# Performance work log

Hardware: AMD Instinct MI355X
Metric: run time of the kernel (lower is better)

## Reference

```python
import jax, jax.numpy as jnp
import numpy as np

B, Cfi, H, W = 2, 32, 192, 192
Cfp, Cfo, NUM = 1, 2, 16
N = H * W
Ct = Cfo + Cfi + Cfi + Cfp  # 67
EPS = 1e-5


def _bn(x, g, b, m, v):
    # x: (B, C, num, N); per-channel inference batchnorm
    inv = g * jax.lax.rsqrt(v + EPS)
    return x * inv[None, :, None, None] + (b - m * inv)[None, :, None, None]


def _pconv(x, Wt):
    # 1x1 conv as channel contraction: Wt (Cout, Cin), x (B, Cin, num, N)
    return jnp.einsum('oc,bcmn->bomn', Wt, x)


def setup_inputs() -> dict:
    key = jax.random.key(0)
    ks = jax.random.split(key, 32)
    inp = {
        'If': jax.random.normal(ks[0], (B, Cfi, H, W), jnp.float32),
        'Pf': jax.random.normal(ks[1], (B, Cfp, H, W), jnp.float32),
        'Ofnum': jax.random.normal(ks[2], (B, Cfo, NUM, N), jnp.float32),
        'args': jax.random.randint(ks[3], (B, NUM, N), 0, N, jnp.int64),
    }
    def conv_w(k, co, ci):
        return jax.random.normal(k, (co, ci), jnp.float32) * (1.0 / np.sqrt(ci))
    def bn_p(k, c):
        k1, k2 = jax.random.split(k)
        return (jnp.ones((c,), jnp.float32),
                jnp.zeros((c,), jnp.float32),
                jax.random.normal(k1, (c,), jnp.float32) * 0.1,
                jax.random.uniform(k2, (c,), jnp.float32, 0.5, 1.5))
    # convXF: Ct->Cfi, Cfi->Cfi (both BN+GELU)
    inp['W1'] = conv_w(ks[4], Cfi, Ct)
    inp['g1'], inp['b1'], inp['m1'], inp['v1'] = bn_p(ks[5], Cfi)
    inp['W2'] = conv_w(ks[6], Cfi, Cfi)
    inp['g2'], inp['b2'], inp['m2'], inp['v2'] = bn_p(ks[7], Cfi)
    # convXL: Cfi->Cfi (BN+GELU), Cfi->Cfi (BN only)
    inp['W3'] = conv_w(ks[8], Cfi, Cfi)
    inp['g3'], inp['b3'], inp['m3'], inp['v3'] = bn_p(ks[9], Cfi)
    inp['W4'] = conv_w(ks[10], Cfi, Cfi)
    inp['g4'], inp['b4'], inp['m4'], inp['v4'] = bn_p(ks[11], Cfi)
    # coef: Cfi -> 3, with bias
    inp['Wc'] = conv_w(ks[12], 3, Cfi)
    inp['bc'] = jax.random.normal(ks[13], (3,), jnp.float32) * 0.01
    return inp


def reference(If, Pf, Ofnum, args,
              W1, g1, b1, m1, v1,
              W2, g2, b2, m2, v2,
              W3, g3, b3, m3, v3,
              W4, g4, b4, m4, v4,
              Wc, bc):
    gelu = lambda x: jax.nn.gelu(x, approximate=False)
    If_flat = If.reshape(B, Cfi, N)   # (B, Cfi, N)
    Pf_flat = Pf.reshape(B, Cfp, N)   # (B, Cfp, M), M == N here

    # per-batch neighbor gather along flattened spatial dim
    gath = jax.vmap(lambda f, a: f[:, a])  # (C,N),(num,N) -> (C,num,N)
    IPfnum = gath(If_flat, args)            # (B, Cfi, num, N)
    Pfnum = gath(Pf_flat, args)             # (B, Cfp, num, N)
    Ifnum = jnp.broadcast_to(If_flat[:, :, None, :], (B, Cfi, NUM, N))

    X = jnp.concatenate([Ifnum, IPfnum, Pfnum, Ofnum], axis=1)  # (B, Ct, num, N)

    h = gelu(_bn(_pconv(X, W1), g1, b1, m1, v1))
    h = gelu(_bn(_pconv(h, W2), g2, b2, m2, v2))
    l = gelu(_bn(_pconv(h, W3), g3, b3, m3, v3))
    l = _bn(_pconv(l, W4), g4, b4, m4, v4)
    XF = gelu(h + l)

    feat = _pconv(XF, Wc) + bc[None, :, None, None]  # (B, 3, num, N)
    Alpha, Beta, Omega = feat[:, 0:1], feat[:, 1:2], feat[:, 2:3]
    Omega = jax.nn.softmax(Omega, axis=2)
    dout = jnp.sum(((Alpha + 1.0) * Pfnum[:, -1:] + Beta) * Omega,
                   axis=2, keepdims=True)  # (B, 1, 1, N)
    return dout.reshape(B, 1, H, W)
```

## Files before the change

### kernel.cpp

```cpp
#include <hip/hip_runtime.h>
#include <math.h>

#define BB   2
#define CFI  32
#define NN   36864
#define NUMM 16

#define ZOFSU (BB * NN * 16)

typedef __attribute__((ext_vector_type(8))) short short8;
typedef __attribute__((ext_vector_type(4))) float f4;
typedef __attribute__((ext_vector_type(16))) float f16v;
typedef __attribute__((ext_vector_type(4))) unsigned uint4v;
typedef __attribute__((ext_vector_type(2))) unsigned u2v;

static __device__ __forceinline__ f16v mm32(short8 a, short8 b, f16v c) {
    return __builtin_amdgcn_mfma_f32_32x32x16_bf16(a, b, c, 0, 0, 0);
}

template <int CTRL>
static __device__ __forceinline__ float dpp_add(float x) {
    int y = __builtin_amdgcn_update_dpp(0, __builtin_bit_cast(int, x),
                                        CTRL, 0xf, 0xf, true);
    return x + __builtin_bit_cast(float, y);
}
template <int CTRL>
static __device__ __forceinline__ float dpp_max(float x) {
    int y = __builtin_amdgcn_update_dpp(0, __builtin_bit_cast(int, x),
                                        CTRL, 0xf, 0xf, true);
    return fmaxf(x, __builtin_bit_cast(float, y));
}

static __device__ __forceinline__ float gelu_fast(float x) {
    const float x2  = x * x;
    const float q   = fmaf(-0.10294310f, x2, -2.30211813f);
    const float e   = exp2f(q * x);
    const float r   = __builtin_amdgcn_rcpf(e + 1.0f);
    return x * r;
}

static __device__ __forceinline__ unsigned bf16_rne_bits(float x) {
    unsigned u = __builtin_bit_cast(unsigned, x);
    return u + 0x7fffu + ((u >> 16) & 1u);
}
static __device__ __forceinline__ void split_pack(float x0, float x1,
                                                  unsigned& hi, unsigned& lo) {
    unsigned r0 = bf16_rne_bits(x0);
    unsigned r1 = bf16_rne_bits(x1);
    float h0 = __builtin_bit_cast(float, r0 & 0xffff0000u);
    float h1 = __builtin_bit_cast(float, r1 & 0xffff0000u);
    hi = (r0 >> 16) | (r1 & 0xffff0000u);
    unsigned s0 = bf16_rne_bits(x0 - h0);
    unsigned s1 = bf16_rne_bits(x1 - h1);
    lo = (s0 >> 16) | (s1 & 0xffff0000u);
}

static __device__ __forceinline__ unsigned pack2(float a, float b) {
    unsigned ua = __builtin_bit_cast(unsigned, a) + 0x8000u;
    unsigned ub = __builtin_bit_cast(unsigned, b) + 0x8000u;
    return (ua >> 16) | (ub & 0xffff0000u);
}
static __device__ __forceinline__ float bflo(unsigned u) {
    return __builtin_bit_cast(float, u << 16);
}
static __device__ __forceinline__ float bfhi(unsigned u) {
    return __builtin_bit_cast(float, u & 0xffff0000u);
}

union UV { unsigned u[4]; short8 v; };

__global__ __launch_bounds__(256) void yz_kernel(
    const float* __restrict__ If, const float* __restrict__ Pf,
    const float* __restrict__ W1, const float* __restrict__ g1,
    const float* __restrict__ b1, const float* __restrict__ m1,
    const float* __restrict__ v1,
    float* __restrict__ wsYZ)
{
    __shared__ float wy[1024], wz[1024], wp[32], bt1[32];
    for (int i = threadIdx.x; i < 1024; i += 256) {
        int o = i >> 5, c = i & 31;
        float inv = g1[o] * rsqrtf(v1[o] + 1e-5f);
        wy[i] = W1[o * 67 + c]      * inv;
        wz[i] = W1[o * 67 + 32 + c] * inv;
    }
    if (threadIdx.x < 32) {
        int o = threadIdx.x;
        float inv = g1[o] * rsqrtf(v1[o] + 1e-5f);
        wp[o]  = W1[o * 67 + 64] * inv;
        bt1[o] = b1[o] - m1[o] * inv;
    }
    __syncthreads();

    const int r  = threadIdx.x & 3;
    const int p  = blockIdx.x * 64 + (threadIdx.x >> 2);
    const int b  = p / NN, n = p - b * NN;
    const int o0 = r * 8;
    const float* ifp = If + (size_t)b * CFI * NN + n;

    float v[32];
#pragma unroll
    for (int c = 0; c < 32; c++) v[c] = ifp[(size_t)c * NN];
    const float pf = Pf[p];

    float accY[8], accZ[8];
#pragma unroll
    for (int j = 0; j < 8; j++) {
        const float4* wyr = (const float4*)&wy[(o0 + j) * 32];
        const float4* wzr = (const float4*)&wz[(o0 + j) * 32];
        float ay = bt1[o0 + j];
        float az = wp[o0 + j] * pf;
#pragma unroll
        for (int c4 = 0; c4 < 8; c4++) {
            float4 a = wyr[c4], z = wzr[c4];
            ay = fmaf(a.x, v[4 * c4 + 0], ay);  az = fmaf(z.x, v[4 * c4 + 0], az);
            ay = fmaf(a.y, v[4 * c4 + 1], ay);  az = fmaf(z.y, v[4 * c4 + 1], az);
            ay = fmaf(a.z, v[4 * c4 + 2], ay);  az = fmaf(z.z, v[4 * c4 + 2], az);
            ay = fmaf(a.w, v[4 * c4 + 3], ay);  az = fmaf(z.w, v[4 * c4 + 3], az);
        }
        accY[j] = ay; accZ[j] = az;
    }

    unsigned* wsu = (unsigned*)wsYZ;
    u2v yA, yB, zA, zB;
    yA[0] = pack2(accY[0], accY[1]); yA[1] = pack2(accY[2], accY[3]);
    yB[0] = pack2(accY[4], accY[5]); yB[1] = pack2(accY[6], accY[7]);
    zA[0] = pack2(accZ[0], accZ[1]); zA[1] = pack2(accZ[2], accZ[3]);
    zB[0] = pack2(accZ[4], accZ[5]); zB[1] = pack2(accZ[6], accZ[7]);
    *(u2v*)(wsu + (size_t)p * 16 + 2 * r)          = yA;
    *(u2v*)(wsu + (size_t)p * 16 + 8 + 2 * r)      = yB;
    *(u2v*)(wsu + ZOFSU + (size_t)p * 16 + 2 * r)     = zA;
    *(u2v*)(wsu + ZOFSU + (size_t)p * 16 + 8 + 2 * r) = zB;
}

#define LOADL(Lc)                                                             \
    {                                                                         \
        A0l = *(const short8*)&wfrag[(Lc)][0][1][lane + io][0];               \
        A0h = *(const short8*)&wfrag[(Lc)][0][0][lane + io][0];               \
        A1l = *(const short8*)&wfrag[(Lc)][1][1][lane + io][0];               \
        A1h = *(const short8*)&wfrag[(Lc)][1][0][lane + io][0];               \
        bq0 = *(const f4*)&btl[(Lc) * 32 +      4 * hi + 4 * io];             \
        bq1 = *(const f4*)&btl[(Lc) * 32 +  8 + 4 * hi + 4 * io];             \
        bq2 = *(const f4*)&btl[(Lc) * 32 + 16 + 4 * hi + 4 * io];             \
        bq3 = *(const f4*)&btl[(Lc) * 32 + 24 + 4 * hi + 4 * io];             \
    }

#define LAYER_MM(ACCV, BIN0, BIN1)                                            \
    {                                                                         \
        ACCV[0]  = bq0[0]; ACCV[1]  = bq0[1]; ACCV[2]  = bq0[2]; ACCV[3]  = bq0[3]; \
        ACCV[4]  = bq1[0]; ACCV[5]  = bq1[1]; ACCV[6]  = bq1[2]; ACCV[7]  = bq1[3]; \
        ACCV[8]  = bq2[0]; ACCV[9]  = bq2[1]; ACCV[10] = bq2[2]; ACCV[11] = bq2[3]; \
        ACCV[12] = bq3[0]; ACCV[13] = bq3[1]; ACCV[14] = bq3[2]; ACCV[15] = bq3[3]; \
        ACCV = mm32(A0l, BIN0.v, ACCV);                                       \
        ACCV = mm32(A0h, BIN0.v, ACCV);                                       \
        ACCV = mm32(A1l, BIN1.v, ACCV);                                       \
        ACCV = mm32(A1h, BIN1.v, ACCV);                                       \
    }

#define GELU_PACK(ACCV, B0V, B1V)                                             \
    {                                                                         \
        _Pragma("unroll")                                                     \
        for (int k = 0; k < 4; k++) {                                         \
            float t0 = gelu_fast(ACCV[2 * k]);                                \
            float t1 = gelu_fast(ACCV[2 * k + 1]);                            \
            B0V.u[k] = pack2(t0, t1);                                         \
            float t2 = gelu_fast(ACCV[8 + 2 * k]);                            \
            float t3 = gelu_fast(ACCV[8 + 2 * k + 1]);                        \
            B1V.u[k] = pack2(t2, t3);                                         \
        }                                                                     \
    }

__global__ __launch_bounds__(256, 5) void main_kernel(
    const float* __restrict__ Pf, const float* __restrict__ Of,
    const int* __restrict__ args,
    const float* __restrict__ W1, const float* __restrict__ g1,
    const float* __restrict__ v1,
    const float* __restrict__ W2, const float* __restrict__ g2,
    const float* __restrict__ b2, const float* __restrict__ m2,
    const float* __restrict__ v2,
    const float* __restrict__ W3, const float* __restrict__ g3,
    const float* __restrict__ b3, const float* __restrict__ m3,
    const float* __restrict__ v3,
    const float* __restrict__ W4, const float* __restrict__ g4,
    const float* __restrict__ b4, const float* __restrict__ m4,
    const float* __restrict__ v4,
    const float* __restrict__ Wc, const float* __restrict__ bc,
    const float* __restrict__ ws, float* __restrict__ out)
{
    __shared__ __align__(16) unsigned wfrag[3][2][2][64][4];
    __shared__ __align__(16) float btl[3 * 32];
    __shared__ __align__(16) float wch[3 * 32];
    __shared__ __align__(16) float w1t[2 * 32];
    __shared__ float bcs[3];
    __shared__ int   izs;

    const float* Ws[3] = {W2, W3, W4};
    const float* gs[3] = {g2, g3, g4};
    const float* vs[3] = {v2, v3, v4};
    const float* bs[3] = {b2, b3, b4};
    const float* ms[3] = {m2, m3, m4};

    for (int idx = threadIdx.x; idx < 1536; idx += 256) {
        int pp  = idx & 3;
        int ln  = (idx >> 2) & 63;
        int kh  = (idx >> 8) & 1;
        int L   = idx >> 9;
        int row = ln & 31;
        int g   = ln >> 5;
        int k   = kh * 16 + 4 * g + 2 * (pp & 1) + 8 * (pp >> 1);
        float inv = gs[L][row] * rsqrtf(vs[L][row] + 1e-5f);
        float w0 = Ws[L][row * 32 + k]     * inv;
        float w1 = Ws[L][row * 32 + k + 1] * inv;
        unsigned hiw, low;
        split_pack(w0, w1, hiw, low);
        wfrag[L][kh][0][ln][pp] = hiw;
        wfrag[L][kh][1][ln][pp] = low;
    }
    if (threadIdx.x < 96) {
        int L = threadIdx.x >> 5, ch = threadIdx.x & 31;
        btl[threadIdx.x] = bs[L][ch] - ms[L][ch] * (gs[L][ch] * rsqrtf(vs[L][ch] + 1e-5f));
        wch[threadIdx.x] = Wc[L * 32 + ch];
    }
    if (threadIdx.x < 64) {
        int t = threadIdx.x >> 5, ch = threadIdx.x & 31;
        float i1 = g1[ch] * rsqrtf(v1[ch] + 1e-5f);
        w1t[threadIdx.x] = W1[ch * 67 + 65 + t] * i1;
    }
    if (threadIdx.x < 3) bcs[threadIdx.x] = bc[threadIdx.x];
    if (threadIdx.x == 0) izs = (int)(args[0] >> 16);
    __syncthreads();

    const unsigned* wsu = (const unsigned*)ws;
    const int lane  = threadIdx.x & 63;
    const int wid   = threadIdx.x >> 6;
    const int m     = lane & 15;
    const int pt    = (lane >> 4) & 1;
    const int hi    = lane >> 5;
    const int q4    = hi << 2;
    const int izero = izs;

    const int base  = blockIdx.x * 32 + wid * 8 + pt;

    uint4v yu0, yu1, zu0, zu1;
    float of0v, of1v, pfg_n;
    int   aI_n;
    {
        const int C0 = base;
        const int b0 = (C0 >= NN) ? 1 : 0;
        const int n0 = C0 - b0 * NN;
        const int a0 = args[(b0 * NUMM + m) * NN + n0];
        of0v = Of[((b0 * 2 + 0) * NUMM + m) * NN + n0];
        of1v = Of[((b0 * 2 + 1) * NUMM + m) * NN + n0];
        pfg_n = Pf[b0 * NN + a0];
        const uint4v* yb = (const uint4v*)(wsu + (size_t)(b0 * NN + n0) * 16 + hi * 8);
        const uint4v* zb = (const uint4v*)(wsu + ZOFSU + (size_t)(b0 * NN + a0) * 16 + hi * 8);
        yu0 = yb[0]; yu1 = yb[1];
        zu0 = zb[0]; zu1 = zb[1];
        const int C1 = (C0 + 2 < BB * NN) ? C0 + 2 : BB * NN - 1;
        const int b1_ = (C1 >= NN) ? 1 : 0;
        const int n1_ = C1 - b1_ * NN;
        aI_n = args[(b1_ * NUMM + m) * NN + n1_];
    }

#pragma unroll 1
    for (int i = 0; i < 4; i++) {
        const int io = i & izero;
        const int C  = base + i * 2;
        const int b  = (C >= NN) ? 1 : 0;
        const int n  = C - b * NN;
        const float pfg = pfg_n;

        short8 A0l, A0h, A1l, A1h;
        f4 bq0, bq1, bq2, bq3;
        LOADL(0);

        UV B0, B1;
#pragma unroll
        for (int q = 0; q < 4; q++) {
            const f4 waq = *(const f4*)&w1t[8 * q + q4 + 4 * io];
            const f4 wbq = *(const f4*)&w1t[32 + 8 * q + q4 + 4 * io];
            const unsigned ya0 = (q < 2) ? yu0[2 * q]     : yu1[2 * q - 4];
            const unsigned ya1 = (q < 2) ? yu0[2 * q + 1] : yu1[2 * q - 3];
            const unsigned za0 = (q < 2) ? zu0[2 * q]     : zu1[2 * q - 4];
            const unsigned za1 = (q < 2) ? zu0[2 * q + 1] : zu1[2 * q - 3];
            float t0 = fmaf(of1v, wbq[0], fmaf(of0v, waq[0], bflo(ya0) + bflo(za0)));
            float t1 = fmaf(of1v, wbq[1], fmaf(of0v, waq[1], bfhi(ya0) + bfhi(za0)));
            float t2 = fmaf(of1v, wbq[2], fmaf(of0v, waq[2], bflo(ya1) + bflo(za1)));
            float t3 = fmaf(of1v, wbq[3], fmaf(of0v, waq[3], bfhi(ya1) + bfhi(za1)));
            t0 = gelu_fast(t0); t1 = gelu_fast(t1);
            t2 = gelu_fast(t2); t3 = gelu_fast(t3);
            const unsigned lo2 = pack2(t0, t1), hi2 = pack2(t2, t3);
            if (q < 2) { B0.u[2 * q] = lo2; B0.u[2 * q + 1] = hi2; }
            else       { B1.u[2 * q - 4] = lo2; B1.u[2 * q - 3] = hi2; }
        }

        {
            const int Cn = (C + 2 < BB * NN) ? C + 2 : BB * NN - 1;
            const int bn = (Cn >= NN) ? 1 : 0;
            const int nn = Cn - bn * NN;
            const uint4v* ybn = (const uint4v*)(wsu + (size_t)(bn * NN + nn) * 16 + hi * 8);
            yu0 = ybn[0]; yu1 = ybn[1];
            of0v = Of[((bn * 2 + 0) * NUMM + m) * NN + nn];
            of1v = Of[((bn * 2 + 1) * NUMM + m) * NN + nn];
            const int aN = aI_n;
            pfg_n = Pf[bn * NN + aN];
            const uint4v* zbn = (const uint4v*)(wsu + ZOFSU + (size_t)(bn * NN + aN) * 16 + hi * 8);
            zu0 = zbn[0]; zu1 = zbn[1];
            const int Ca = (C + 4 < BB * NN) ? C + 4 : BB * NN - 1;
            const int ba = (Ca >= NN) ? 1 : 0;
            const int na = Ca - ba * NN;
            aI_n = args[(ba * NUMM + m) * NN + na];
        }

        f16v acc;
        LAYER_MM(acc, B0, B1);
        LOADL(1);
        UV P0, P1;
        GELU_PACK(acc, P0, P1);
        B0 = P0; B1 = P1;

        LAYER_MM(acc, B0, B1);
        LOADL(2);
        GELU_PACK(acc, B0, B1);

        LAYER_MM(acc, B0, B1);

        float pa = 0.0f, pb = 0.0f, po = 0.0f;
#pragma unroll
        for (int q = 0; q < 4; q++) {
            const f4 wAq = *(const f4*)&wch[      8 * q + q4 + 4 * io];
            const f4 wBq = *(const f4*)&wch[32 +  8 * q + q4 + 4 * io];
            const f4 wOq = *(const f4*)&wch[64 +  8 * q + q4 + 4 * io];
            const unsigned pu0 = (q < 2) ? P0.u[2 * q]     : P1.u[2 * q - 4];
            const unsigned pu1 = (q < 2) ? P0.u[2 * q + 1] : P1.u[2 * q - 3];
            const float h20 = bflo(pu0), h21 = bfhi(pu0);
            const float h22 = bflo(pu1), h23 = bfhi(pu1);
            float xf0 = gelu_fast(h20 + acc[4 * q + 0]);
            float xf1 = gelu_fast(h21 + acc[4 * q + 1]);
            float xf2 = gelu_fast(h22 + acc[4 * q + 2]);
            float xf3 = gelu_fast(h23 + acc[4 * q + 3]);
            pa = fmaf(wAq[0], xf0, pa); pa = fmaf(wAq[1], xf1, pa);
            pa = fmaf(wAq[2], xf2, pa); pa = fmaf(wAq[3], xf3, pa);
            pb = fmaf(wBq[0], xf0, pb); pb = fmaf(wBq[1], xf1, pb);
            pb = fmaf(wBq[2], xf2, pb); pb = fmaf(wBq[3], xf3, pb);
            po = fmaf(wOq[0], xf0, po); po = fmaf(wOq[1], xf1, po);
            po = fmaf(wOq[2], xf2, po); po = fmaf(wOq[3], xf3, po);
        }
        pa += __shfl_xor(pa, 32, 64);
        pb += __shfl_xor(pb, 32, 64);
        po += __shfl_xor(po, 32, 64);

        const float alpha = pa + bcs[0];
        const float beta_ = pb + bcs[1];
        const float omega = po + bcs[2];
        const float val = fmaf(alpha + 1.0f, pfg, beta_);

        float mx = dpp_max<0xB1>(omega);
        mx = dpp_max<0x4E>(mx);
        mx = dpp_max<0x141>(mx);
        mx = dpp_max<0x140>(mx);
        const float e = __expf(omega - mx);
        float S = e, T = val * e;
        S = dpp_add<0xB1>(S);   T = dpp_add<0xB1>(T);
        S = dpp_add<0x4E>(S);   T = dpp_add<0x4E>(T);
        S = dpp_add<0x141>(S);  T = dpp_add<0x141>(T);
        S = dpp_add<0x140>(S);  T = dpp_add<0x140>(T);

        if ((lane & 15) == 0 && lane < 32)
            out[b * NN + n] = T * __builtin_amdgcn_rcpf(S);
    }
}

extern "C" void kernel_launch(void* const* d_in, const int* in_sizes, int n_in,
                              void* d_out, int out_size, void* d_ws, size_t ws_size,
                              hipStream_t stream) {
    const float* If    = (const float*)d_in[0];
    const float* Pf    = (const float*)d_in[1];
    const float* Of    = (const float*)d_in[2];
    const int*   args  = (const int*)d_in[3];
    const float* W1    = (const float*)d_in[4];
    const float* g1    = (const float*)d_in[5];
    const float* b1    = (const float*)d_in[6];
    const float* m1    = (const float*)d_in[7];
    const float* v1    = (const float*)d_in[8];
    const float* W2    = (const float*)d_in[9];
    const float* g2    = (const float*)d_in[10];
    const float* b2    = (const float*)d_in[11];
    const float* m2    = (const float*)d_in[12];
    const float* v2    = (const float*)d_in[13];
    const float* W3    = (const float*)d_in[14];
    const float* g3    = (const float*)d_in[15];
    const float* b3    = (const float*)d_in[16];
    const float* m3    = (const float*)d_in[17];
    const float* v3    = (const float*)d_in[18];
    const float* W4    = (const float*)d_in[19];
    const float* g4    = (const float*)d_in[20];
    const float* b4    = (const float*)d_in[21];
    const float* m4    = (const float*)d_in[22];
    const float* v4    = (const float*)d_in[23];
    const float* Wc    = (const float*)d_in[24];
    const float* bc    = (const float*)d_in[25];

    float* ws  = (float*)d_ws;
    float* out = (float*)d_out;

    yz_kernel<<<(BB * NN) / 64, 256, 0, stream>>>(
        If, Pf, W1, g1, b1, m1, v1, ws);

    main_kernel<<<(BB * NN) / 32, 256, 0, stream>>>(
        Pf, Of, args,
        W1, g1, v1,
        W2, g2, b2, m2, v2,
        W3, g3, b3, m3, v3,
        W4, g4, b4, m4, v4,
        Wc, bc, ws, out);
}
```

Before: 225.7 us.

## Split layer-1 gather and GELU into separate kernel writing bf16 activations to workspace

Adds an h1_kernel that performs the neighbor gather (args, Of, Pf, Y/Z partial sums), applies the first layer's GELU, and writes the packed bf16 h1 activations plus the gathered Pf to workspace. A new main_kernel2 then streams these contiguous activations instead of doing the scattered gather inline. The goal is to take the irregular gather latency out of the MFMA-heavy main kernel. In exchange it adds an extra launch and a large write and read-back of h1 (about 4.7MB each way). It falls back to the old fused path when the workspace is too small.

```diff
diff --git a/kernel.cpp b/kernel.cpp
--- a/kernel.cpp
+++ b/kernel.cpp
@@ -7,6 +7,10 @@
 #define NUMM 16
 
 #define ZOFSU (BB * NN * 16)
+#define H1OFS (2 * BB * NN * 16)
+#define H1SZ  (BB * NN * 16 * 16)
+#define PFOFS (H1OFS + H1SZ)
+#define WS_NEEDED_BYTES ((size_t)(PFOFS + BB * NN * 16) * 4)
 
 typedef __attribute__((ext_vector_type(8))) short short8;
 typedef __attribute__((ext_vector_type(4))) float f4;
@@ -132,6 +136,70 @@
     *(u2v*)(wsu + ZOFSU + (size_t)p * 16 + 8 + 2 * r) = zB;
 }
 
+__global__ __launch_bounds__(256) void h1_kernel(
+    const float* __restrict__ Pf, const float* __restrict__ Of,
+    const int* __restrict__ args,
+    const float* __restrict__ W1, const float* __restrict__ g1,
+    const float* __restrict__ v1,
+    float* __restrict__ wsF)
+{
+    __shared__ float w1a[32], w1b[32];
+    if (threadIdx.x < 64) {
+        int t = threadIdx.x >> 5, ch = threadIdx.x & 31;
+        float i1 = g1[ch] * rsqrtf(v1[ch] + 1e-5f);
+        float w = W1[ch * 67 + 65 + t] * i1;
+        if (t == 0) w1a[ch] = w; else w1b[ch] = w;
+    }
+    __syncthreads();
+
+    unsigned* wsu = (unsigned*)wsF;
+    const int m = threadIdx.x & 15;
+    const int p = blockIdx.x * 16 + (threadIdx.x >> 4);
+    const int b = (p >= NN) ? 1 : 0;
+    const int n = p - b * NN;
+
+    const int   a   = args[(b * NUMM + m) * NN + n];
+    const float of0 = Of[((b * 2 + 0) * NUMM + m) * NN + n];
+    const float of1 = Of[((b * 2 + 1) * NUMM + m) * NN + n];
+    const float pfg = Pf[b * NN + a];
+
+    const uint4v* yb = (const uint4v*)(wsu + (size_t)p * 16);
+    const uint4v* zb = (const uint4v*)(wsu + ZOFSU + (size_t)(b * NN + a) * 16);
+    uint4v yv0 = yb[0], yv1 = yb[1], yv2 = yb[2], yv3 = yb[3];
+    uint4v zv0 = zb[0], zv1 = zb[1], zv2 = zb[2], zv3 = zb[3];
+
+    unsigned outv[16];
+#pragma unroll
+    for (int u = 0; u < 16; u += 2) {
+        const int hi = u >> 3, q = (u & 7) >> 1;
+        const int c  = 8 * q + 4 * hi;
+        const f4 wa = *(const f4*)&w1a[c];
+        const f4 wb = *(const f4*)&w1b[c];
+        const unsigned yu0 = (u < 4) ? yv0[u & 3] : (u < 8) ? yv1[u & 3]
+                           : (u < 12) ? yv2[u & 3] : yv3[u & 3];
+        const unsigned yu1 = ((u + 1) < 4) ? yv0[(u + 1) & 3] : ((u + 1) < 8) ? yv1[(u + 1) & 3]
+                           : ((u + 1) < 12) ? yv2[(u + 1) & 3] : yv3[(u + 1) & 3];
+        const unsigned zu0 = (u < 4) ? zv0[u & 3] : (u < 8) ? zv1[u & 3]
+                           : (u < 12) ? zv2[u & 3] : zv3[u & 3];
+        const unsigned zu1 = ((u + 1) < 4) ? zv0[(u + 1) & 3] : ((u + 1) < 8) ? zv1[(u + 1) & 3]
+                           : ((u + 1) < 12) ? zv2[(u + 1) & 3] : zv3[(u + 1) & 3];
+        float x0 = fmaf(of1, wb[0], fmaf(of0, wa[0], bflo(yu0) + bflo(zu0)));
+        float x1 = fmaf(of1, wb[1], fmaf(of0, wa[1], bfhi(yu0) + bfhi(zu0)));
+        float x2 = fmaf(of1, wb[2], fmaf(of0, wa[2], bflo(yu1) + bflo(zu1)));
+        float x3 = fmaf(of1, wb[3], fmaf(of0, wa[3], bfhi(yu1) + bfhi(zu1)));
+        outv[u]     = pack2(gelu_fast(x0), gelu_fast(x1));
+        outv[u + 1] = pack2(gelu_fast(x2), gelu_fast(x3));
+    }
+
+    uint4v* op = (uint4v*)(wsu + H1OFS + ((size_t)p * 16 + m) * 16);
+    uint4v o0, o1, o2, o3;
+#pragma unroll
+    for (int k = 0; k < 4; k++) { o0[k] = outv[k]; o1[k] = outv[4 + k];
+                                  o2[k] = outv[8 + k]; o3[k] = outv[12 + k]; }
+    op[0] = o0; op[1] = o1; op[2] = o2; op[3] = o3;
+    wsF[PFOFS + (size_t)p * 16 + m] = pfg;
+}
+
 #define LOADL(Lc)                                                             \
     {                                                                         \
         A0l = *(const short8*)&wfrag[(Lc)][0][1][lane + io][0];               \
@@ -168,6 +236,160 @@
             B1V.u[k] = pack2(t2, t3);                                         \
         }                                                                     \
     }
+
+#define MAIN_PROLOGUE                                                         \
+    const float* Ws[3] = {W2, W3, W4};                                        \
+    const float* gs[3] = {g2, g3, g4};                                        \
+    const float* vs[3] = {v2, v3, v4};                                        \
+    const float* bs[3] = {b2, b3, b4};                                        \
+    const float* ms[3] = {m2, m3, m4};                                        \
+    for (int idx = threadIdx.x; idx < 1536; idx += 256) {                     \
+        int pp  = idx & 3;                                                    \
+        int ln  = (idx >> 2) & 63;                                            \
+        int kh  = (idx >> 8) & 1;                                             \
+        int L   = idx >> 9;                                                   \
+        int row = ln & 31;                                                    \
+        int g   = ln >> 5;                                                    \
+        int k   = kh * 16 + 4 * g + 2 * (pp & 1) + 8 * (pp >> 1);             \
+        float inv = gs[L][row] * rsqrtf(vs[L][row] + 1e-5f);                  \
+        float w0 = Ws[L][row * 32 + k]     * inv;                             \
+        float w1 = Ws[L][row * 32 + k + 1] * inv;                             \
+        unsigned hiw, low;                                                    \
+        split_pack(w0, w1, hiw, low);                                         \
+        wfrag[L][kh][0][ln][pp] = hiw;                                        \
+        wfrag[L][kh][1][ln][pp] = low;                                        \
+    }                                                                         \
+    if (threadIdx.x < 96) {                                                   \
+        int L = threadIdx.x >> 5, ch = threadIdx.x & 31;                      \
+        btl[threadIdx.x] = bs[L][ch] - ms[L][ch] * (gs[L][ch] * rsqrtf(vs[L][ch] + 1e-5f)); \
+        wch[threadIdx.x] = Wc[L * 32 + ch];                                   \
+    }                                                                         \
+    if (threadIdx.x < 3) bcs[threadIdx.x] = bc[threadIdx.x];
+
+__global__ __launch_bounds__(256, 5) void main_kernel2(
+    const int* __restrict__ args,
+    const float* __restrict__ W2, const float* __restrict__ g2,
+    const float* __restrict__ b2, const float* __restrict__ m2,
+    const float* __restrict__ v2,
+    const float* __restrict__ W3, const float* __restrict__ g3,
+    const float* __restrict__ b3, const float* __restrict__ m3,
+    const float* __restrict__ v3,
+    const float* __restrict__ W4, const float* __restrict__ g4,
+    const float* __restrict__ b4, const float* __restrict__ m4,
+    const float* __restrict__ v4,
+    const float* __restrict__ Wc, const float* __restrict__ bc,
+    const float* __restrict__ ws, float* __restrict__ out)
+{
+    __shared__ __align__(16) unsigned wfrag[3][2][2][64][4];
+    __shared__ __align__(16) float btl[3 * 32];
+    __shared__ __align__(16) float wch[3 * 32];
+    __shared__ float bcs[3];
+    __shared__ int   izs;
+
+    MAIN_PROLOGUE
+    if (threadIdx.x == 0) izs = (int)(args[0] >> 16);
+    __syncthreads();
+
+    const unsigned* wsu = (const unsigned*)ws;
+    const unsigned* h1g = wsu + H1OFS;
+    const float*    pff = ws + PFOFS;
+    const int lane  = threadIdx.x & 63;
+    const int wid   = threadIdx.x >> 6;
+    const int m     = lane & 15;
+    const int pt    = (lane >> 4) & 1;
+    const int hi    = lane >> 5;
+    const int q4    = hi << 2;
+    const int izero = izs;
+
+    const int base  = blockIdx.x * 32 + wid * 8 + pt;
+
+    uint4v h0c, h1c;
+    float pfg_n;
+    {
+        const unsigned* hp = h1g + ((size_t)base * 16 + m) * 16 + hi * 8;
+        h0c = *(const uint4v*)hp;
+        h1c = *(const uint4v*)(hp + 4);
+        pfg_n = pff[(size_t)base * 16 + m];
+    }
+
+#pragma unroll 1
+    for (int i = 0; i < 4; i++) {
+        const int io = i & izero;
+        const int C  = base + i * 2;
+        const float pfg = pfg_n;
+
+        short8 A0l, A0h, A1l, A1h;
+        f4 bq0, bq1, bq2, bq3;
+        LOADL(0);
+
+        UV B0, B1;
+#pragma unroll
+        for (int k = 0; k < 4; k++) { B0.u[k] = h0c[k]; B1.u[k] = h1c[k]; }
+
+        {
+            const int Cn = (C + 2 < BB * NN) ? C + 2 : BB * NN - 1;
+            const unsigned* hp = h1g + ((size_t)Cn * 16 + m) * 16 + hi * 8;
+            h0c = *(const uint4v*)hp;
+            h1c = *(const uint4v*)(hp + 4);
+            pfg_n = pff[(size_t)Cn * 16 + m];
+        }
+
+        f16v acc;
+        LAYER_MM(acc, B0, B1);
+        LOADL(1);
+        UV P0, P1;
+        GELU_PACK(acc, P0, P1);
+        B0 = P0; B1 = P1;
+
+        LAYER_MM(acc, B0, B1);
+        LOADL(2);
+        GELU_PACK(acc, B0, B1);
+
+        LAYER_MM(acc, B0, B1);
+
+        float pa = 0.0f, pb = 0.0f, po = 0.0f;
+#pragma unroll
+        for (int q = 0; q < 4; q++) {
+            const f4 wAq = *(const f4*)&wch[      8 * q + q4 + 4 * io];
+            const f4 wBq = *(const f4*)&wch[32 +  8 * q + q4 + 4 * io];
+            const f4 wOq = *(const f4*)&wch[64 +  8 * q + q4 + 4 * io];
+            const unsigned pu0 = (q < 2) ? P0.u[2 * q]     : P1.u[2 * q - 4];
+            const unsigned pu1 = (q < 2) ? P0.u[2 * q + 1] : P1.u[2 * q - 3];
+            float xf0 = gelu_fast(bflo(pu0) + acc[4 * q + 0]);
+            float xf1 = gelu_fast(bfhi(pu0) + acc[4 * q + 1]);
+            float xf2 = gelu_fast(bflo(pu1) + acc[4 * q + 2]);
+            float xf3 = gelu_fast(bfhi(pu1) + acc[4 * q + 3]);
+            pa = fmaf(wAq[0], xf0, pa); pa = fmaf(wAq[1], xf1, pa);
+            pa = fmaf(wAq[2], xf2, pa); pa = fmaf(wAq[3], xf3, pa);
+            pb = fmaf(wBq[0], xf0, pb); pb = fmaf(wBq[1], xf1, pb);
+            pb = fmaf(wBq[2], xf2, pb); pb = fmaf(wBq[3], xf3, pb);
+            po = fmaf(wOq[0], xf0, po); po = fmaf(wOq[1], xf1, po);
+            po = fmaf(wOq[2], xf2, po); po = fmaf(wOq[3], xf3, po);
+        }
+        pa += __shfl_xor(pa, 32, 64);
+        pb += __shfl_xor(pb, 32, 64);
+        po += __shfl_xor(po, 32, 64);
+
+        const float alpha = pa + bcs[0];
+        const float beta_ = pb + bcs[1];
+        const float omega = po + bcs[2];
+        const float val = fmaf(alpha + 1.0f, pfg, beta_);
+
+        float mx = dpp_max<0xB1>(omega);
+        mx = dpp_max<0x4E>(mx);
+        mx = dpp_max<0x141>(mx);
+        mx = dpp_max<0x140>(mx);
+        const float e = __expf(omega - mx);
+        float S = e, T = val * e;
+        S = dpp_add<0xB1>(S);   T = dpp_add<0xB1>(T);
+        S = dpp_add<0x4E>(S);   T = dpp_add<0x4E>(T);
+        S = dpp_add<0x141>(S);  T = dpp_add<0x141>(T);
+        S = dpp_add<0x140>(S);  T = dpp_add<0x140>(T);
+
+        if ((lane & 15) == 0 && lane < 32)
+            out[C] = T * __builtin_amdgcn_rcpf(S);
+    }
+}
 
 __global__ __launch_bounds__(256, 5) void main_kernel(
     const float* __restrict__ Pf, const float* __restrict__ Of,
@@ -193,39 +415,12 @@
     __shared__ float bcs[3];
     __shared__ int   izs;
 
-    const float* Ws[3] = {W2, W3, W4};
-    const float* gs[3] = {g2, g3, g4};
-    const float* vs[3] = {v2, v3, v4};
-    const float* bs[3] = {b2, b3, b4};
-    const float* ms[3] = {m2, m3, m4};
-
-    for (int idx = threadIdx.x; idx < 1536; idx += 256) {
-        int pp  = idx & 3;
-        int ln  = (idx >> 2) & 63;
-        int kh  = (idx >> 8) & 1;
-        int L   = idx >> 9;
-        int row = ln & 31;
-        int g   = ln >> 5;
-        int k   = kh * 16 + 4 * g + 2 * (pp & 1) + 8 * (pp >> 1);
-        float inv = gs[L][row] * rsqrtf(vs[L][row] + 1e-5f);
-        float w0 = Ws[L][row * 32 + k]     * inv;
-        float w1 = Ws[L][row * 32 + k + 1] * inv;
-        unsigned hiw, low;
-        split_pack(w0, w1, hiw, low);
-        wfrag[L][kh][0][ln][pp] = hiw;
-        wfrag[L][kh][1][ln][pp] = low;
-    }
-    if (threadIdx.x < 96) {
-        int L = threadIdx.x >> 5, ch = threadIdx.x & 31;
-        btl[threadIdx.x] = bs[L][ch] - ms[L][ch] * (gs[L][ch] * rsqrtf(vs[L][ch] + 1e-5f));
-        wch[threadIdx.x] = Wc[L * 32 + ch];
-    }
+    MAIN_PROLOGUE
     if (threadIdx.x < 64) {
         int t = threadIdx.x >> 5, ch = threadIdx.x & 31;
         float i1 = g1[ch] * rsqrtf(v1[ch] + 1e-5f);
         w1t[threadIdx.x] = W1[ch * 67 + 65 + t] * i1;
     }
-    if (threadIdx.x < 3) bcs[threadIdx.x] = bc[threadIdx.x];
     if (threadIdx.x == 0) izs = (int)(args[0] >> 16);
     __syncthreads();
 
@@ -332,12 +527,10 @@
             const f4 wOq = *(const f4*)&wch[64 +  8 * q + q4 + 4 * io];
             const unsigned pu0 = (q < 2) ? P0.u[2 * q]     : P1.u[2 * q - 4];
             const unsigned pu1 = (q < 2) ? P0.u[2 * q + 1] : P1.u[2 * q - 3];
-            const float h20 = bflo(pu0), h21 = bfhi(pu0);
-            const float h22 = bflo(pu1), h23 = bfhi(pu1);
-            float xf0 = gelu_fast(h20 + acc[4 * q + 0]);
-            float xf1 = gelu_fast(h21 + acc[4 * q + 1]);
-            float xf2 = gelu_fast(h22 + acc[4 * q + 2]);
-            float xf3 = gelu_fast(h23 + acc[4 * q + 3]);
+            float xf0 = gelu_fast(bflo(pu0) + acc[4 * q + 0]);
+            float xf1 = gelu_fast(bfhi(pu0) + acc[4 * q + 1]);
+            float xf2 = gelu_fast(bflo(pu1) + acc[4 * q + 2]);
+            float xf3 = gelu_fast(bfhi(pu1) + acc[4 * q + 3]);
             pa = fmaf(wAq[0], xf0, pa); pa = fmaf(wAq[1], xf1, pa);
             pa = fmaf(wAq[2], xf2, pa); pa = fmaf(wAq[3], xf3, pa);
             pb = fmaf(wBq[0], xf0, pb); pb = fmaf(wBq[1], xf1, pb);
@@ -406,11 +599,22 @@
     yz_kernel<<<(BB * NN) / 64, 256, 0, stream>>>(
         If, Pf, W1, g1, b1, m1, v1, ws);
 
-    main_kernel<<<(BB * NN) / 32, 256, 0, stream>>>(
-        Pf, Of, args,
-        W1, g1, v1,
-        W2, g2, b2, m2, v2,
-        W3, g3, b3, m3, v3,
-        W4, g4, b4, m4, v4,
-        Wc, bc, ws, out);
-}
+    if (ws_size >= WS_NEEDED_BYTES) {
+        h1_kernel<<<(BB * NN) / 16, 256, 0, stream>>>(
+            Pf, Of, args, W1, g1, v1, ws);
+        main_kernel2<<<(BB * NN) / 32, 256, 0, stream>>>(
+            args,
+            W2, g2, b2, m2, v2,
+            W3, g3, b3, m3, v3,
+            W4, g4, b4, m4, v4,
+            Wc, bc, ws, out);
+    } else {
+        main_kernel<<<(BB * NN) / 32, 256, 0, stream>>>(
+            Pf, Of, args,
+            W1, g1, v1,
+            W2, g2, b2, m2, v2,
+            W3, g3, b3, m3, v3,
+            W4, g4, b4, m4, v4,
+            Wc, bc, ws, out);
+    }
+}
```

After: 245.1 us. 1.09x slower.

## Split first-layer gather and GELU into a separate kernel staging bf16 activations

Applied to the files above, without the earlier changes.

Adds an h1_kernel that gathers the Y/Z partial sums, Of and Pf per neighbor, applies the first layer's BN and GELU, and writes packed bf16 activations plus the gathered Pf values to workspace. The main kernel then reads these precomputed activations instead of doing the irregular gathers and layer-1 math inline. It also runs at a higher occupancy hint (6) and loads bias values inside the layer macro. The aim is to lighten the MFMA kernel and cut its register pressure. In exchange it adds a large workspace write and re-read of the intermediate activations, and it relies on the workspace being big enough, which is never checked.

```diff
diff --git a/kernel.cpp b/kernel.cpp
--- a/kernel.cpp
+++ b/kernel.cpp
@@ -7,6 +7,10 @@
 #define NUMM 16
 
 #define ZOFSU (BB * NN * 16)
+#define H1OFS (2 * BB * NN * 16)
+#define H1SZ  (BB * NN * 16 * 16)
+#define PFOFS (H1OFS + H1SZ)
+#define WS_NEEDED_BYTES ((size_t)(PFOFS + BB * NN * 16) * 4)
 
 typedef __attribute__((ext_vector_type(8))) short short8;
 typedef __attribute__((ext_vector_type(4))) float f4;
@@ -132,24 +136,80 @@
     *(u2v*)(wsu + ZOFSU + (size_t)p * 16 + 8 + 2 * r) = zB;
 }
 
+__global__ __launch_bounds__(256) void h1_kernel(
+    const float* __restrict__ Pf, const float* __restrict__ Of,
+    const int* __restrict__ args,
+    const float* __restrict__ W1, const float* __restrict__ g1,
+    const float* __restrict__ v1,
+    float* __restrict__ wsF)
+{
+    __shared__ float w1a[32], w1b[32];
+    if (threadIdx.x < 64) {
+        int t = threadIdx.x >> 5, ch = threadIdx.x & 31;
+        float i1 = g1[ch] * rsqrtf(v1[ch] + 1e-5f);
+        float w = W1[ch * 67 + 65 + t] * i1;
+        if (t == 0) w1a[ch] = w; else w1b[ch] = w;
+    }
+    __syncthreads();
+
+    unsigned* wsu = (unsigned*)wsF;
+    const int qd = threadIdx.x & 3;
+    const int m  = (threadIdx.x >> 2) & 15;
+    const int p  = blockIdx.x * 4 + (threadIdx.x >> 6);
+    const int b  = (p >= NN) ? 1 : 0;
+    const int n  = p - b * NN;
+
+    const int   a   = args[(b * NUMM + m) * NN + n];
+    const float of0 = Of[((b * 2 + 0) * NUMM + m) * NN + n];
+    const float of1 = Of[((b * 2 + 1) * NUMM + m) * NN + n];
+
+    const uint4v y16 = *(const uint4v*)(wsu + (size_t)p * 16 + qd * 4);
+    const uint4v z16 = *(const uint4v*)(wsu + ZOFSU + (size_t)(b * NN + a) * 16 + qd * 4);
+
+    const int c_a = (qd & 1) * 16 + (qd >> 1) * 4;
+    const f4 waA = *(const f4*)&w1a[c_a];
+    const f4 wbA = *(const f4*)&w1b[c_a];
+    const f4 waB = *(const f4*)&w1a[c_a + 8];
+    const f4 wbB = *(const f4*)&w1b[c_a + 8];
+
+    float x0 = fmaf(of1, wbA[0], fmaf(of0, waA[0], bflo(y16[0]) + bflo(z16[0])));
+    float x1 = fmaf(of1, wbA[1], fmaf(of0, waA[1], bfhi(y16[0]) + bfhi(z16[0])));
+    float x2 = fmaf(of1, wbA[2], fmaf(of0, waA[2], bflo(y16[1]) + bflo(z16[1])));
+    float x3 = fmaf(of1, wbA[3], fmaf(of0, waA[3], bfhi(y16[1]) + bfhi(z16[1])));
+    float x4 = fmaf(of1, wbB[0], fmaf(of0, waB[0], bflo(y16[2]) + bflo(z16[2])));
+    float x5 = fmaf(of1, wbB[1], fmaf(of0, waB[1], bfhi(y16[2]) + bfhi(z16[2])));
+    float x6 = fmaf(of1, wbB[2], fmaf(of0, waB[2], bflo(y16[3]) + bflo(z16[3])));
+    float x7 = fmaf(of1, wbB[3], fmaf(of0, waB[3], bfhi(y16[3]) + bfhi(z16[3])));
+
+    uint4v o;
+    o[0] = pack2(gelu_fast(x0), gelu_fast(x1));
+    o[1] = pack2(gelu_fast(x2), gelu_fast(x3));
+    o[2] = pack2(gelu_fast(x4), gelu_fast(x5));
+    o[3] = pack2(gelu_fast(x6), gelu_fast(x7));
+
+    *(uint4v*)(wsu + H1OFS + ((size_t)p * 16 + m) * 16 + qd * 4) = o;
+    if (qd == 0) wsF[PFOFS + (size_t)p * 16 + m] = Pf[b * NN + a];
+}
+
 #define LOADL(Lc)                                                             \
     {                                                                         \
         A0l = *(const short8*)&wfrag[(Lc)][0][1][lane + io][0];               \
         A0h = *(const short8*)&wfrag[(Lc)][0][0][lane + io][0];               \
         A1l = *(const short8*)&wfrag[(Lc)][1][1][lane + io][0];               \
         A1h = *(const short8*)&wfrag[(Lc)][1][0][lane + io][0];               \
-        bq0 = *(const f4*)&btl[(Lc) * 32 +      4 * hi + 4 * io];             \
-        bq1 = *(const f4*)&btl[(Lc) * 32 +  8 + 4 * hi + 4 * io];             \
-        bq2 = *(const f4*)&btl[(Lc) * 32 + 16 + 4 * hi + 4 * io];             \
-        bq3 = *(const f4*)&btl[(Lc) * 32 + 24 + 4 * hi + 4 * io];             \
-    }
-
-#define LAYER_MM(ACCV, BIN0, BIN1)                                            \
+    }
+
+#define LAYER_MM(Lc, ACCV, BIN0, BIN1)                                        \
     {                                                                         \
-        ACCV[0]  = bq0[0]; ACCV[1]  = bq0[1]; ACCV[2]  = bq0[2]; ACCV[3]  = bq0[3]; \
-        ACCV[4]  = bq1[0]; ACCV[5]  = bq1[1]; ACCV[6]  = bq1[2]; ACCV[7]  = bq1[3]; \
-        ACCV[8]  = bq2[0]; ACCV[9]  = bq2[1]; ACCV[10] = bq2[2]; ACCV[11] = bq2[3]; \
-        ACCV[12] = bq3[0]; ACCV[13] = bq3[1]; ACCV[14] = bq3[2]; ACCV[15] = bq3[3]; \
+        f4 t_;                                                                \
+        t_ = *(const f4*)&btl[(Lc) * 32 +      4 * hi + 4 * io];              \
+        ACCV[0]  = t_[0]; ACCV[1]  = t_[1]; ACCV[2]  = t_[2]; ACCV[3]  = t_[3]; \
+        t_ = *(const f4*)&btl[(Lc) * 32 +  8 + 4 * hi + 4 * io];              \
+        ACCV[4]  = t_[0]; ACCV[5]  = t_[1]; ACCV[6]  = t_[2]; ACCV[7]  = t_[3]; \
+        t_ = *(const f4*)&btl[(Lc) * 32 + 16 + 4 * hi + 4 * io];              \
+        ACCV[8]  = t_[0]; ACCV[9]  = t_[1]; ACCV[10] = t_[2]; ACCV[11] = t_[3]; \
+        t_ = *(const f4*)&btl[(Lc) * 32 + 24 + 4 * hi + 4 * io];              \
+        ACCV[12] = t_[0]; ACCV[13] = t_[1]; ACCV[14] = t_[2]; ACCV[15] = t_[3]; \
         ACCV = mm32(A0l, BIN0.v, ACCV);                                       \
         ACCV = mm32(A0h, BIN0.v, ACCV);                                       \
         ACCV = mm32(A1l, BIN1.v, ACCV);                                       \
@@ -169,11 +229,8 @@
         }                                                                     \
     }
 
-__global__ __launch_bounds__(256, 5) void main_kernel(
-    const float* __restrict__ Pf, const float* __restrict__ Of,
+__global__ __launch_bounds__(256, 6) void main_kernel2(
     const int* __restrict__ args,
-    const float* __restrict__ W1, const float* __restrict__ g1,
-    const float* __restrict__ v1,
     const float* __restrict__ W2, const float* __restrict__ g2,
     const float* __restrict__ b2, const float* __restrict__ m2,
     const float* __restrict__ v2,
@@ -189,7 +246,6 @@
     __shared__ __align__(16) unsigned wfrag[3][2][2][64][4];
     __shared__ __align__(16) float btl[3 * 32];
     __shared__ __align__(16) float wch[3 * 32];
-    __shared__ __align__(16) float w1t[2 * 32];
     __shared__ float bcs[3];
     __shared__ int   izs;
 
@@ -220,16 +276,13 @@
         btl[threadIdx.x] = bs[L][ch] - ms[L][ch] * (gs[L][ch] * rsqrtf(vs[L][ch] + 1e-5f));
         wch[threadIdx.x] = Wc[L * 32 + ch];
     }
-    if (threadIdx.x < 64) {
-        int t = threadIdx.x >> 5, ch = threadIdx.x & 31;
-        float i1 = g1[ch] * rsqrtf(v1[ch] + 1e-5f);
-        w1t[threadIdx.x] = W1[ch * 67 + 65 + t] * i1;
-    }
     if (threadIdx.x < 3) bcs[threadIdx.x] = bc[threadIdx.x];
     if (threadIdx.x == 0) izs = (int)(args[0] >> 16);
     __syncthreads();
 
     const unsigned* wsu = (const unsigned*)ws;
+    const unsigned* h1g = wsu + H1OFS;
+    const float*    pff = ws + PFOFS;
     const int lane  = threadIdx.x & 63;
     const int wid   = threadIdx.x >> 6;
     const int m     = lane & 15;
@@ -240,89 +293,48 @@
 
     const int base  = blockIdx.x * 32 + wid * 8 + pt;
 
-    uint4v yu0, yu1, zu0, zu1;
-    float of0v, of1v, pfg_n;
-    int   aI_n;
+    uint4v h0c, h1c;
+    float pfg_n;
     {
-        const int C0 = base;
-        const int b0 = (C0 >= NN) ? 1 : 0;
-        const int n0 = C0 - b0 * NN;
-        const int a0 = args[(b0 * NUMM + m) * NN + n0];
-        of0v = Of[((b0 * 2 + 0) * NUMM + m) * NN + n0];
-        of1v = Of[((b0 * 2 + 1) * NUMM + m) * NN + n0];
-        pfg_n = Pf[b0 * NN + a0];
-        const uint4v* yb = (const uint4v*)(wsu + (size_t)(b0 * NN + n0) * 16 + hi * 8);
-        const uint4v* zb = (const uint4v*)(wsu + ZOFSU + (size_t)(b0 * NN + a0) * 16 + hi * 8);
-        yu0 = yb[0]; yu1 = yb[1];
-        zu0 = zb[0]; zu1 = zb[1];
-        const int C1 = (C0 + 2 < BB * NN) ? C0 + 2 : BB * NN - 1;
-        const int b1_ = (C1 >= NN) ? 1 : 0;
-        const int n1_ = C1 - b1_ * NN;
-        aI_n = args[(b1_ * NUMM + m) * NN + n1_];
+        const unsigned* hp = h1g + ((size_t)base * 16 + m) * 16 + hi * 8;
+        h0c = *(const uint4v*)hp;
+        h1c = *(const uint4v*)(hp + 4);
+        pfg_n = pff[(size_t)base * 16 + m];
     }
 
 #pragma unroll 1
     for (int i = 0; i < 4; i++) {
         const int io = i & izero;
         const int C  = base + i * 2;
-        const int b  = (C >= NN) ? 1 : 0;
-        const int n  = C - b * NN;
         const float pfg = pfg_n;
 
         short8 A0l, A0h, A1l, A1h;
-        f4 bq0, bq1, bq2, bq3;
         LOADL(0);
 
         UV B0, B1;
 #pragma unroll
-        for (int q = 0; q < 4; q++) {
-            const f4 waq = *(const f4*)&w1t[8 * q + q4 + 4 * io];
-            const f4 wbq = *(const f4*)&w1t[32 + 8 * q + q4 + 4 * io];
-            const unsigned ya0 = (q < 2) ? yu0[2 * q]     : yu1[2 * q - 4];
-            const unsigned ya1 = (q < 2) ? yu0[2 * q + 1] : yu1[2 * q - 3];
-            const unsigned za0 = (q < 2) ? zu0[2 * q]     : zu1[2 * q - 4];
-            const unsigned za1 = (q < 2) ? zu0[2 * q + 1] : zu1[2 * q - 3];
-            float t0 = fmaf(of1v, wbq[0], fmaf(of0v, waq[0], bflo(ya0) + bflo(za0)));
-            float t1 = fmaf(of1v, wbq[1], fmaf(of0v, waq[1], bfhi(ya0) + bfhi(za0)));
-            float t2 = fmaf(of1v, wbq[2], fmaf(of0v, waq[2], bflo(ya1) + bflo(za1)));
-            float t3 = fmaf(of1v, wbq[3], fmaf(of0v, waq[3], bfhi(ya1) + bfhi(za1)));
-            t0 = gelu_fast(t0); t1 = gelu_fast(t1);
-            t2 = gelu_fast(t2); t3 = gelu_fast(t3);
-            const unsigned lo2 = pack2(t0, t1), hi2 = pack2(t2, t3);
-            if (q < 2) { B0.u[2 * q] = lo2; B0.u[2 * q + 1] = hi2; }
-            else       { B1.u[2 * q - 4] = lo2; B1.u[2 * q - 3] = hi2; }
-        }
+        for (int k = 0; k < 4; k++) { B0.u[k] = h0c[k]; B1.u[k] = h1c[k]; }
 
         {
             const int Cn = (C + 2 < BB * NN) ? C + 2 : BB * NN - 1;
-            const int bn = (Cn >= NN) ? 1 : 0;
-            const int nn = Cn - bn * NN;
-            const uint4v* ybn = (const uint4v*)(wsu + (size_t)(bn * NN + nn) * 16 + hi * 8);
-            yu0 = ybn[0]; yu1 = ybn[1];
-            of0v = Of[((bn * 2 + 0) * NUMM + m) * NN + nn];
-            of1v = Of[((bn * 2 + 1) * NUMM + m) * NN + nn];
-            const int aN = aI_n;
-            pfg_n = Pf[bn * NN + aN];
-            const uint4v* zbn = (const uint4v*)(wsu + ZOFSU + (size_t)(bn * NN + aN) * 16 + hi * 8);
-            zu0 = zbn[0]; zu1 = zbn[1];
-            const int Ca = (C + 4 < BB * NN) ? C + 4 : BB * NN - 1;
-            const int ba = (Ca >= NN) ? 1 : 0;
-            const int na = Ca - ba * NN;
-            aI_n = args[(ba * NUMM + m) * NN + na];
+            const unsigned* hp = h1g + ((size_t)Cn * 16 + m) * 16 + hi * 8;
+            h0c = *(const uint4v*)hp;
+            h1c = *(const uint4v*)(hp + 4);
+            pfg_n = pff[(size_t)Cn * 16 + m];
         }
 
         f16v acc;
-        LAYER_MM(acc, B0, B1);
+        LAYER_MM(0, acc, B0, B1);
         LOADL(1);
         UV P0, P1;
         GELU_PACK(acc, P0, P1);
         B0 = P0; B1 = P1;
 
-        LAYER_MM(acc, B0, B1);
+        LAYER_MM(1, acc, B0, B1);
         LOADL(2);
         GELU_PACK(acc, B0, B1);
 
-        LAYER_MM(acc, B0, B1);
+        LAYER_MM(2, acc, B0, B1);
 
         float pa = 0.0f, pb = 0.0f, po = 0.0f;
 #pragma unroll
@@ -332,12 +344,10 @@
             const f4 wOq = *(const f4*)&wch[64 +  8 * q + q4 + 4 * io];
             const unsigned pu0 = (q < 2) ? P0.u[2 * q]     : P1.u[2 * q - 4];
             const unsigned pu1 = (q < 2) ? P0.u[2 * q + 1] : P1.u[2 * q - 3];
-            const float h20 = bflo(pu0), h21 = bfhi(pu0);
-            const float h22 = bflo(pu1), h23 = bfhi(pu1);
-            float xf0 = gelu_fast(h20 + acc[4 * q + 0]);
-            float xf1 = gelu_fast(h21 + acc[4 * q + 1]);
-            float xf2 = gelu_fast(h22 + acc[4 * q + 2]);
-            float xf3 = gelu_fast(h23 + acc[4 * q + 3]);
+            float xf0 = gelu_fast(bflo(pu0) + acc[4 * q + 0]);
+            float xf1 = gelu_fast(bfhi(pu0) + acc[4 * q + 1]);
+            float xf2 = gelu_fast(bflo(pu1) + acc[4 * q + 2]);
+            float xf3 = gelu_fast(bfhi(pu1) + acc[4 * q + 3]);
             pa = fmaf(wAq[0], xf0, pa); pa = fmaf(wAq[1], xf1, pa);
             pa = fmaf(wAq[2], xf2, pa); pa = fmaf(wAq[3], xf3, pa);
             pb = fmaf(wBq[0], xf0, pb); pb = fmaf(wBq[1], xf1, pb);
@@ -366,7 +376,7 @@
         S = dpp_add<0x140>(S);  T = dpp_add<0x140>(T);
 
         if ((lane & 15) == 0 && lane < 32)
-            out[b * NN + n] = T * __builtin_amdgcn_rcpf(S);
+            out[C] = T * __builtin_amdgcn_rcpf(S);
     }
 }
 
@@ -406,9 +416,11 @@
     yz_kernel<<<(BB * NN) / 64, 256, 0, stream>>>(
         If, Pf, W1, g1, b1, m1, v1, ws);
 
-    main_kernel<<<(BB * NN) / 32, 256, 0, stream>>>(
-        Pf, Of, args,
-        W1, g1, v1,
+    h1_kernel<<<(BB * NN) / 4, 256, 0, stream>>>(
+        Pf, Of, args, W1, g1, v1, ws);
+
+    main_kernel2<<<(BB * NN) / 32, 256, 0, stream>>>(
+        args,
         W2, g2, b2, m2, v2,
         W3, g3, b3, m3, v3,
         W4, g4, b4, m4, v4,
```

After: 245.0 us. +8.5%, slower.
